# Kernel optimization log

Hardware: AMD Instinct MI355X
Metric: run time of the kernel (lower is better)

Reference implementation:

```python
import jax, jax.numpy as jnp
import numpy as np

H = 16
D_MODEL = 1024
D_K = D_MODEL // H


def setup_inputs() -> dict:
    key = jax.random.key(0)
    ks = jax.random.split(key, 11)
    B, S = 2, 2048
    scale = 1.0 / np.sqrt(D_MODEL)
    inp = {
        "query": jax.random.normal(ks[0], (B, S, D_MODEL), dtype=jnp.float32),
        "key": jax.random.normal(ks[1], (B, S, D_MODEL), dtype=jnp.float32),
        "value": jax.random.normal(ks[2], (B, S, D_MODEL), dtype=jnp.float32),
        "Wq": jax.random.normal(ks[3], (D_MODEL, D_MODEL), dtype=jnp.float32) * scale,
        "bq": jnp.zeros((D_MODEL,), dtype=jnp.float32),
        "Wk": jax.random.normal(ks[4], (D_MODEL, D_MODEL), dtype=jnp.float32) * scale,
        "bk": jnp.zeros((D_MODEL,), dtype=jnp.float32),
        "Wv": jax.random.normal(ks[5], (D_MODEL, D_MODEL), dtype=jnp.float32) * scale,
        "bv": jnp.zeros((D_MODEL,), dtype=jnp.float32),
        "Wo": jax.random.normal(ks[6], (D_MODEL, D_MODEL), dtype=jnp.float32) * scale,
        "bo": jnp.zeros((D_MODEL,), dtype=jnp.float32),
    }
    return inp


def _mha(query, key, value, Wq, bq, Wk, bk, Wv, bv, Wo, bo):
    B, S, _ = query.shape
    # linear projections (torch nn.Linear: x @ W.T + b)
    q = query @ Wq.T + bq
    k = key @ Wk.T + bk
    v = value @ Wv.T + bv
    # split heads: [B, S, D] -> [B, H, S, d_k]
    q = q.reshape(B, S, H, D_K).transpose(0, 2, 1, 3)
    k = k.reshape(B, S, H, D_K).transpose(0, 2, 1, 3)
    v = v.reshape(B, S, H, D_K).transpose(0, 2, 1, 3)
    # scaled dot-product attention with manual stable softmax
    scores = jnp.einsum("bhqd,bhkd->bhqk", q, k) / jnp.sqrt(jnp.float32(D_K))
    stable = scores - jnp.max(scores, axis=-1, keepdims=True)
    e = jnp.exp(stable)
    attn = e / jnp.sum(e, axis=-1, keepdims=True)
    ctx = jnp.einsum("bhqk,bhkd->bhqd", attn, v)
    # merge heads and final projection
    ctx = ctx.transpose(0, 2, 1, 3).reshape(B, S, H * D_K)
    return ctx @ Wo.T + bo


def reference(query, key, value, Wq, bq, Wk, bk, Wv, bv, Wo, bo):
    return _mha(query, key, value, Wq, bq, Wk, bk, Wv, bv, Wo, bo)
```

## Files before the change

kernel.cpp:

```cpp
#include <hip/hip_runtime.h>


#define S_LEN 2048
#define BATCH 2
#define DM    1024
#define NH    16
#define DKH   64
#define BS    (BATCH * S_LEN)

typedef _Float16 f16x8 __attribute__((ext_vector_type(8)));
typedef _Float16 f16x4 __attribute__((ext_vector_type(4)));
typedef _Float16 f16x2 __attribute__((ext_vector_type(2)));
typedef __fp16   h16x2 __attribute__((ext_vector_type(2)));
typedef float    f32x4 __attribute__((ext_vector_type(4)));
typedef float    f32x16 __attribute__((ext_vector_type(16)));

__device__ __forceinline__ f16x2 pk_f16(float a, float b) {
  h16x2 r = __builtin_amdgcn_cvt_pkrtz(a, b);
  return __builtin_bit_cast(f16x2, r);
}

__device__ __forceinline__ void gld16(const void* g, void* l) {
  __builtin_amdgcn_global_load_lds(
      (const __attribute__((address_space(1))) void*)g,
      (__attribute__((address_space(3))) void*)l, 16, 0, 0);
}

__device__ __forceinline__ float fast_exp2(float x) {
#if __has_builtin(__builtin_amdgcn_exp2f)
  return __builtin_amdgcn_exp2f(x);
#else
  return exp2f(x);
#endif
}

__device__ __forceinline__ int swap23(int x) {
  return (x & ~12) | ((x & 4) << 1) | ((x & 8) >> 1);
}

__global__ __launch_bounds__(256) void cvt_all(
    const float* __restrict__ q, const float* __restrict__ k, const float* __restrict__ v,
    const float* __restrict__ wq, const float* __restrict__ wk,
    const float* __restrict__ wv, const float* __restrict__ wo,
    _Float16* __restrict__ xq, _Float16* __restrict__ xk, _Float16* __restrict__ xv,
    _Float16* __restrict__ w16)
{
  const int y = blockIdx.y;
  const float* src; _Float16* dst; int n;
  if (y == 0)      { src = q;  dst = xq; n = BS * DM; }
  else if (y == 1) { src = k;  dst = xk; n = BS * DM; }
  else if (y == 2) { src = v;  dst = xv; n = BS * DM; }
  else {
    src = (y == 3) ? wq : ((y == 4) ? wk : ((y == 5) ? wv : wo));
    dst = w16 + (size_t)(y - 3) * (DM * DM);
    n = DM * DM;
  }
  int i0 = (blockIdx.x * 256 + threadIdx.x) * 4;
  if (i0 < n) {
    float4 f = *(const float4*)(src + i0);
    f16x2 lo = pk_f16(f.x, f.y);
    f16x2 hi = pk_f16(f.z, f.w);
    f16x4 hh; hh[0] = lo[0]; hh[1] = lo[1]; hh[2] = hi[0]; hh[3] = hi[1];
    *(f16x4*)(dst + i0) = hh;
  }
}

template <typename OUT_T, bool VT>
__device__ __forceinline__ void gemm_core(
    const _Float16* __restrict__ A, const _Float16* __restrict__ W,
    const float* __restrict__ bias, OUT_T* __restrict__ out, float oscale)
{
  const int tid  = threadIdx.x;
  const int l    = tid & 63;
  const int wv   = tid >> 6;
  const int c    = l & 15, quad = l >> 4;
  const int m0   = blockIdx.y * 128, n0 = blockIdx.x * 128;
  const int wm   = wv & 1, wn = wv >> 1;
  __shared__ _Float16 sA[128 * 64];
  __shared__ _Float16 sB[128 * 64];

  const _Float16* gA[4]; const _Float16* gB[4];
#pragma unroll
  for (int p = 0; p < 4; ++p) {
    int s = tid + p * 256, r = s >> 3, g = (s & 7) ^ (r & 7);
    gA[p] = A + (size_t)(m0 + r) * DM + g * 8;
    gB[p] = W + (size_t)(n0 + r) * DM + g * 8;
  }
  const int cx = c & 7;

  f32x4 acc[4][4] = {};
  for (int k0 = 0; k0 < DM; k0 += 64) {
    __syncthreads();
#pragma unroll
    for (int p = 0; p < 4; ++p) {
      gld16(gA[p] + k0, sA + (tid + p * 256) * 8);
      gld16(gB[p] + k0, sB + (tid + p * 256) * 8);
    }
    __syncthreads();
#pragma unroll
    for (int ks = 0; ks < 2; ++ks) {
      f16x8 af[4], bf[4];
#pragma unroll
      for (int i = 0; i < 4; ++i)
        af[i] = *(const f16x8*)&sA[(wm * 64 + i * 16 + c) * 64 + ((ks * 4 + quad) ^ cx) * 8];
#pragma unroll
      for (int j = 0; j < 4; ++j)
        bf[j] = *(const f16x8*)&sB[(wn * 64 + j * 16 + c) * 64 + ((ks * 4 + quad) ^ cx) * 8];
#pragma unroll
      for (int i = 0; i < 4; ++i)
#pragma unroll
        for (int j = 0; j < 4; ++j)
          acc[i][j] = __builtin_amdgcn_mfma_f32_16x16x32_f16(af[i], bf[j], acc[i][j], 0, 0, 0);
    }
  }
  if constexpr (VT) {
#pragma unroll
    for (int j = 0; j < 4; ++j) {
      int col = n0 + wn * 64 + j * 16 + c;
      float bb = bias[col];
      int hh = col >> 6, dd = col & 63;
#pragma unroll
      for (int i = 0; i < 4; ++i) {
        int row = m0 + wm * 64 + i * 16 + quad * 4;
        int bb2 = row >> 11, ss = row & (S_LEN - 1);
        _Float16* dst = (_Float16*)out + ((size_t)(bb2 * NH + hh) * DKH + dd) * S_LEN + ss;
        f16x4 v4;
#pragma unroll
        for (int r = 0; r < 4; ++r) v4[r] = (_Float16)((acc[i][j][r] + bb) * oscale);
        *(f16x4*)dst = v4;
      }
    }
  } else {
#pragma unroll
    for (int j = 0; j < 4; ++j) {
      int col = n0 + wn * 64 + j * 16 + c;
      float bb = bias[col];
#pragma unroll
      for (int i = 0; i < 4; ++i) {
        int row = m0 + wm * 64 + i * 16 + quad * 4;
#pragma unroll
        for (int r = 0; r < 4; ++r) {
          float vv = (acc[i][j][r] + bb) * oscale;
          out[(size_t)(row + r) * DM + col] = (OUT_T)vv;
        }
      }
    }
  }
}

#define SC_Q (0.125f * 1.44269504088896340736f)

__global__ __launch_bounds__(256) void proj3(
    const _Float16* __restrict__ xq, const _Float16* __restrict__ xk,
    const _Float16* __restrict__ xv, const _Float16* __restrict__ w16,
    const float* __restrict__ bq, const float* __restrict__ bk, const float* __restrict__ bv,
    _Float16* __restrict__ Q, _Float16* __restrict__ K, _Float16* __restrict__ Vt)
{
  const int z = blockIdx.z;
  if (z == 2) {
    gemm_core<_Float16, true>(xv, w16 + (size_t)2 * DM * DM, bv, Vt, 1.0f);
  } else if (z == 0) {
    gemm_core<_Float16, false>(xq, w16, bq, Q, SC_Q);
  } else {
    gemm_core<_Float16, false>(xk, w16 + (size_t)DM * DM, bk, K, 1.0f);
  }
}

__global__ __launch_bounds__(256) void out_gemm(
    const _Float16* __restrict__ ctx, const _Float16* __restrict__ wo,
    const float* __restrict__ bo, float* __restrict__ out)
{
  gemm_core<float, false>(ctx, wo, bo, out, 1.0f);
}

__global__ __launch_bounds__(256, 2) void attn(
    const _Float16* __restrict__ Q, const _Float16* __restrict__ K,
    const _Float16* __restrict__ Vt, _Float16* __restrict__ ctx)
{
  const int tid = threadIdx.x;
  const int l   = tid & 63, wv = tid >> 6;
  const int lo5 = l & 31, hf = l >> 5;
  const int q0  = blockIdx.x * 128;
  const int bh  = blockIdx.y;
  const int b   = bh >> 4, hd = bh & 15;
  __shared__ _Float16 sK[2][64 * 64];
  __shared__ _Float16 sV[2][64 * 64];

  f16x8 qf[4];
  {
    const _Float16* Qg = Q + ((size_t)(b * S_LEN + q0 + wv * 32 + lo5)) * DM + hd * DKH + 8 * hf;
#pragma unroll
    for (int kc = 0; kc < 4; ++kc) qf[kc] = *(const f16x8*)(Qg + 16 * kc);
  }

  f32x16 o[2] = {};
  float l_part = 0.f;
  const f16x2 ones = {(_Float16)1.0f, (_Float16)1.0f};

  const _Float16* Kg0 = K + ((size_t)b * S_LEN) * DM + hd * DKH;
  const _Float16* Vg0 = Vt + ((size_t)bh * DKH) * S_LEN;

  const int sa = tid,       ra = sa >> 3, ba = (sa & 7) ^ (ra & 7);
  const int sb = tid + 256, rb = sb >> 3, bb = (sb & 7) ^ (rb & 7);
  const _Float16* gKa = Kg0 + (size_t)swap23(ra) * DM + ba * 8;
  const _Float16* gKb = Kg0 + (size_t)swap23(rb) * DM + bb * 8;
  const _Float16* gVa = Vg0 + (size_t)ra * S_LEN + ba * 8;
  const _Float16* gVb = Vg0 + (size_t)rb * S_LEN + bb * 8;
  const int rx = lo5 & 7;

  gld16(gKa, sK[0] + sa * 8);
  gld16(gKb, sK[0] + sb * 8);
  gld16(gVa, sV[0] + sa * 8);
  gld16(gVb, sV[0] + sb * 8);
  __syncthreads();

  for (int kt = 0; kt < S_LEN / 64; ++kt) {
    const int cur = kt & 1;
    const int nk = (kt < S_LEN / 64 - 1) ? (kt + 1) : kt;
    const size_t k0n = (size_t)nk * 64;
    gld16(gKa + k0n * DM, sK[cur ^ 1] + sa * 8);
    gld16(gKb + k0n * DM, sK[cur ^ 1] + sb * 8);
    gld16(gVa + k0n,      sV[cur ^ 1] + sa * 8);
    gld16(gVb + k0n,      sV[cur ^ 1] + sb * 8);

    f32x16 sAcc[2] = {};
#pragma unroll
    for (int kb = 0; kb < 2; ++kb)
#pragma unroll
      for (int kc = 0; kc < 4; ++kc) {
        f16x8 kf = *(const f16x8*)&sK[cur][(32 * kb + lo5) * 64 + ((2 * kc + hf) ^ rx) * 8];
        sAcc[kb] = __builtin_amdgcn_mfma_f32_32x32x16_f16(kf, qf[kc], sAcc[kb], 0, 0, 0);
      }

    f16x8 pPv[2][2];
#pragma unroll
    for (int kb = 0; kb < 2; ++kb)
#pragma unroll
      for (int half = 0; half < 2; ++half)
#pragma unroll
        for (int j2 = 0; j2 < 4; ++j2) {
          float p0 = fast_exp2(sAcc[kb][8 * half + 2 * j2]);
          float p1 = fast_exp2(sAcc[kb][8 * half + 2 * j2 + 1]);
          f16x2 pk = pk_f16(p0, p1);
          pPv[kb][half][2 * j2]     = pk[0];
          pPv[kb][half][2 * j2 + 1] = pk[1];
          l_part = __builtin_amdgcn_fdot2(__builtin_bit_cast(h16x2, pk),
                                          __builtin_bit_cast(h16x2, ones), l_part, false);
        }

#pragma unroll
    for (int db = 0; db < 2; ++db)
#pragma unroll
      for (int kc2 = 0; kc2 < 4; ++kc2) {
        f16x8 vf = *(const f16x8*)&sV[cur][(32 * db + lo5) * 64 + ((2 * kc2 + hf) ^ rx) * 8];
        o[db] = __builtin_amdgcn_mfma_f32_32x32x16_f16(pPv[kc2 >> 1][kc2 & 1], vf, o[db], 0, 0, 0);
      }

    __syncthreads();
  }

  l_part += __shfl_xor(l_part, 32);
  float* lsum = (float*)&sK[0][0] + wv * 32;
  if (hf == 0) lsum[lo5] = l_part;
  float inv[16];
#pragma unroll
  for (int r = 0; r < 16; ++r) {
    int qq = 8 * (r >> 2) + 4 * hf + (r & 3);
    inv[r] = 1.0f / lsum[qq];
  }

  _Float16* Og = ctx + ((size_t)(b * S_LEN + q0 + wv * 32)) * DM + hd * DKH;
#pragma unroll
  for (int db = 0; db < 2; ++db)
#pragma unroll
    for (int r = 0; r < 16; ++r) {
      int qq = 8 * (r >> 2) + 4 * hf + (r & 3);
      Og[(size_t)qq * DM + 32 * db + lo5] = (_Float16)(o[db][r] * inv[r]);
    }
}

extern "C" void kernel_launch(void* const* d_in, const int* in_sizes, int n_in,
                              void* d_out, int out_size, void* d_ws, size_t ws_size,
                              hipStream_t stream)
{
  (void)in_sizes; (void)n_in; (void)out_size; (void)ws_size;
  const float* q  = (const float*)d_in[0];
  const float* k  = (const float*)d_in[1];
  const float* v  = (const float*)d_in[2];
  const float* wq = (const float*)d_in[3];
  const float* bq = (const float*)d_in[4];
  const float* wk = (const float*)d_in[5];
  const float* bk = (const float*)d_in[6];
  const float* wv = (const float*)d_in[7];
  const float* bv = (const float*)d_in[8];
  const float* wo = (const float*)d_in[9];
  const float* bo = (const float*)d_in[10];

  char* ws = (char*)d_ws;
  _Float16* XQ  = (_Float16*)(ws);
  _Float16* XK  = (_Float16*)(ws + (8u  << 20));
  _Float16* XV  = (_Float16*)(ws + (16u << 20));
  _Float16* W16 = (_Float16*)(ws + (24u << 20));
  _Float16* Qp  = (_Float16*)(ws + (32u << 20));
  _Float16* Kp  = (_Float16*)(ws + (40u << 20));
  _Float16* VT  = (_Float16*)(ws + (48u << 20));
  _Float16* CTX = XQ;
  float* out = (float*)d_out;

  cvt_all<<<dim3(4096, 7), 256, 0, stream>>>(q, k, v, wq, wk, wv, wo, XQ, XK, XV, W16);
  proj3<<<dim3(8, 32, 3), 256, 0, stream>>>(XQ, XK, XV, W16, bq, bk, bv, Qp, Kp, VT);
  attn<<<dim3(16, 32), 256, 0, stream>>>(Qp, Kp, VT, CTX);
  out_gemm<<<dim3(8, 32), 256, 0, stream>>>(CTX, W16 + (size_t)3 * DM * DM, bo, out);
}
```

Before: 226.5 us.

## Halve attention block size and map head blocks to XCDs for L2 reuse

Each attention block now covers 64 queries with 2 waves instead of 128 queries with 4 waves, so 1024 blocks are launched on a 1D grid. The block index is remapped so that all query tiles of one (batch, head) land on the same XCD, which keeps K/V reads within that XCD's L2. Each thread now issues four K and four V async loads per tile, and the redundant final-iteration prefetch is skipped. The smaller blocks double the number of K/V tile loads into LDS per query, and occupancy depends on LDS use per block.

```diff
diff --git a/kernel.cpp b/kernel.cpp
--- a/kernel.cpp
+++ b/kernel.cpp
@@ -173,15 +173,17 @@
   gemm_core<float, false>(ctx, wo, bo, out, 1.0f);
 }
 
-__global__ __launch_bounds__(256, 2) void attn(
+__global__ __launch_bounds__(128, 2) void attn(
     const _Float16* __restrict__ Q, const _Float16* __restrict__ K,
     const _Float16* __restrict__ Vt, _Float16* __restrict__ ctx)
 {
   const int tid = threadIdx.x;
   const int l   = tid & 63, wv = tid >> 6;
   const int lo5 = l & 31, hf = l >> 5;
-  const int q0  = blockIdx.x * 128;
-  const int bh  = blockIdx.y;
+  const int id  = blockIdx.x;
+  const int xcd = id & 7, j = id >> 3;
+  const int bh  = xcd * 4 + (j >> 5);
+  const int q0  = (j & 31) * 64;
   const int b   = bh >> 4, hd = bh & 15;
   __shared__ _Float16 sK[2][64 * 64];
   __shared__ _Float16 sV[2][64 * 64];
@@ -200,28 +202,35 @@
   const _Float16* Kg0 = K + ((size_t)b * S_LEN) * DM + hd * DKH;
   const _Float16* Vg0 = Vt + ((size_t)bh * DKH) * S_LEN;
 
-  const int sa = tid,       ra = sa >> 3, ba = (sa & 7) ^ (ra & 7);
-  const int sb = tid + 256, rb = sb >> 3, bb = (sb & 7) ^ (rb & 7);
-  const _Float16* gKa = Kg0 + (size_t)swap23(ra) * DM + ba * 8;
-  const _Float16* gKb = Kg0 + (size_t)swap23(rb) * DM + bb * 8;
-  const _Float16* gVa = Vg0 + (size_t)ra * S_LEN + ba * 8;
-  const _Float16* gVb = Vg0 + (size_t)rb * S_LEN + bb * 8;
+  const _Float16* gK[4]; const _Float16* gV[4];
+  int ls[4];
+#pragma unroll
+  for (int p = 0; p < 4; ++p) {
+    int s = tid + p * 128, r = s >> 3, g = (s & 7) ^ (r & 7);
+    gK[p] = Kg0 + (size_t)swap23(r) * DM + g * 8;
+    gV[p] = Vg0 + (size_t)r * S_LEN + g * 8;
+    ls[p] = s * 8;
+  }
   const int rx = lo5 & 7;
 
-  gld16(gKa, sK[0] + sa * 8);
-  gld16(gKb, sK[0] + sb * 8);
-  gld16(gVa, sV[0] + sa * 8);
-  gld16(gVb, sV[0] + sb * 8);
+#pragma unroll
+  for (int p = 0; p < 4; ++p) {
+    gld16(gK[p], sK[0] + ls[p]);
+    gld16(gV[p], sV[0] + ls[p]);
+  }
   __syncthreads();
 
   for (int kt = 0; kt < S_LEN / 64; ++kt) {
     const int cur = kt & 1;
-    const int nk = (kt < S_LEN / 64 - 1) ? (kt + 1) : kt;
-    const size_t k0n = (size_t)nk * 64;
-    gld16(gKa + k0n * DM, sK[cur ^ 1] + sa * 8);
-    gld16(gKb + k0n * DM, sK[cur ^ 1] + sb * 8);
-    gld16(gVa + k0n,      sV[cur ^ 1] + sa * 8);
-    gld16(gVb + k0n,      sV[cur ^ 1] + sb * 8);
+    if (kt < S_LEN / 64 - 1) {
+#pragma unroll
+      for (int p = 0; p < 4; ++p) {
+        gK[p] += 64 * DM;
+        gV[p] += 64;
+        gld16(gK[p], sK[cur ^ 1] + ls[p]);
+        gld16(gV[p], sV[cur ^ 1] + ls[p]);
+      }
+    }
 
     f32x16 sAcc[2] = {};
 #pragma unroll
@@ -309,6 +318,6 @@
 
   cvt_all<<<dim3(4096, 7), 256, 0, stream>>>(q, k, v, wq, wk, wv, wo, XQ, XK, XV, W16);
   proj3<<<dim3(8, 32, 3), 256, 0, stream>>>(XQ, XK, XV, W16, bq, bk, bv, Qp, Kp, VT);
-  attn<<<dim3(16, 32), 256, 0, stream>>>(Qp, Kp, VT, CTX);
+  attn<<<dim3(1024), 128, 0, stream>>>(Qp, Kp, VT, CTX);
   out_gemm<<<dim3(8, 32), 256, 0, stream>>>(CTX, W16 + (size_t)3 * DM * DM, bo, out);
 }
```

Result: slower. 237.5 us (+4.9%).
